# Kernel tuning notes

Measured on AMD Instinct MI355X. Metric: run time of the kernel, lower is better.

## Reference

```python
import jax, jax.numpy as jnp
import numpy as np
import math

BS, N, D_MODEL, H = 8, 1024, 512, 8
D_K = D_MODEL // H


def setup_inputs() -> dict:
    key = jax.random.key(0)
    ks = jax.random.split(key, 12)
    s = 1.0 / math.sqrt(D_MODEL)
    inp = {
        "query": jax.random.normal(ks[0], (BS, N, D_MODEL), jnp.float32),
        "key": jax.random.normal(ks[1], (BS, N, D_MODEL), jnp.float32),
        "value": jax.random.normal(ks[2], (BS, N, D_MODEL), jnp.float32),
        "wc_matrix": jax.random.normal(ks[3], (BS, N, N), jnp.float32),
        "Wq": jax.random.normal(ks[4], (D_MODEL, D_MODEL), jnp.float32) * s,
        "bq": jnp.zeros((D_MODEL,), jnp.float32),
        "Wk": jax.random.normal(ks[5], (D_MODEL, D_MODEL), jnp.float32) * s,
        "bk": jnp.zeros((D_MODEL,), jnp.float32),
        "Wv": jax.random.normal(ks[6], (D_MODEL, D_MODEL), jnp.float32) * s,
        "bv": jnp.zeros((D_MODEL,), jnp.float32),
        "Wo": jax.random.normal(ks[7], (D_MODEL, D_MODEL), jnp.float32) * s,
        "bo": jnp.zeros((D_MODEL,), jnp.float32),
    }
    return inp


def _split_heads(x):
    # (bs, N, d_model) -> (bs, h, N, d_k)
    b, n, _ = x.shape
    return x.reshape(b, n, H, D_K).transpose(0, 2, 1, 3)


def reference(query, key, value, wc_matrix, Wq, bq, Wk, bk, Wv, bv, Wo, bo):
    # Linear projections (torch Linear: x @ W.T + b), split into heads
    q = _split_heads(query @ Wq.T + bq)
    k = _split_heads(key @ Wk.T + bk)
    v = _split_heads(value @ Wv.T + bv)

    # scores: (bs, h, N, N)
    scores = jnp.einsum("bhnd,bhmd->bhnm", q, k) / jnp.sqrt(jnp.float32(D_K))
    # WC modulation: scores * softmax(wc)[:, None] + scores  (softmax_wc=True, residual=True)
    wc_sm = jax.nn.softmax(wc_matrix, axis=-1)[:, None]  # (bs, 1, N, N)
    scores = scores * wc_sm + scores
    p_attn = jax.nn.softmax(scores, axis=-1)  # dropout is identity in eval

    a = jnp.einsum("bhnm,bhmd->bhnd", p_attn, v)
    a = a.transpose(0, 2, 1, 3).reshape(query.shape[0], -1, D_MODEL)
    return a @ Wo.T + bo
```

## Files before the change

### kernel.cpp

```cpp
#include <hip/hip_runtime.h>
#include <math.h>


#define BS 8
#define SEQ 1024
#define DM 512
#define NH 8
#define DK 64
#define ROWS (BS * SEQ)

typedef __bf16 bf16_t;
typedef bf16_t bf16x8 __attribute__((ext_vector_type(8)));
typedef bf16_t bf16x4 __attribute__((ext_vector_type(4)));
typedef float f32x4 __attribute__((ext_vector_type(4)));

__device__ inline f32x4 mfma32(bf16x8 a, bf16x8 b, f32x4 c) {
  return __builtin_amdgcn_mfma_f32_16x16x32_bf16(a, b, c, 0, 0, 0);
}

__device__ inline bf16x8 cvt8(float4 a, float4 b) {
  bf16x8 r;
  r[0] = (bf16_t)a.x; r[1] = (bf16_t)a.y; r[2] = (bf16_t)a.z; r[3] = (bf16_t)a.w;
  r[4] = (bf16_t)b.x; r[5] = (bf16_t)b.y; r[6] = (bf16_t)b.z; r[7] = (bf16_t)b.w;
  return r;
}

__global__ __launch_bounds__(256) void wc_softmax_kernel(const float* __restrict__ wc,
                                                         bf16_t* __restrict__ G) {
  int row = blockIdx.x;
  const float* x = wc + (size_t)row * SEQ;
  bf16_t* y = G + (size_t)row * SEQ;
  int t = threadIdx.x;
  float4 v = *(const float4*)(x + t * 4);
  float m = fmaxf(fmaxf(v.x, v.y), fmaxf(v.z, v.w));
#pragma unroll
  for (int off = 32; off > 0; off >>= 1) m = fmaxf(m, __shfl_xor(m, off, 64));
  __shared__ float sm[4], ss[4];
  int w = t >> 6;
  if ((t & 63) == 0) sm[w] = m;
  __syncthreads();
  m = fmaxf(fmaxf(sm[0], sm[1]), fmaxf(sm[2], sm[3]));
  float4 e;
  e.x = __expf(v.x - m); e.y = __expf(v.y - m);
  e.z = __expf(v.z - m); e.w = __expf(v.w - m);
  float s = e.x + e.y + e.z + e.w;
#pragma unroll
  for (int off = 32; off > 0; off >>= 1) s += __shfl_xor(s, off, 64);
  if ((t & 63) == 0) ss[w] = s;
  __syncthreads();
  s = ss[0] + ss[1] + ss[2] + ss[3];
  float inv = 1.0f / s;
  bf16x4 g;
  g[0] = (bf16_t)(1.0f + e.x * inv);
  g[1] = (bf16_t)(1.0f + e.y * inv);
  g[2] = (bf16_t)(1.0f + e.z * inv);
  g[3] = (bf16_t)(1.0f + e.w * inv);
  *(bf16x4*)(y + t * 4) = g;
}

__global__ __launch_bounds__(256) void gemm_qkv_kernel(
    const float* xq, const float* xk, const float* xv,
    const float* Wq, const float* Wk, const float* Wv,
    const float* bq, const float* bk, const float* bv,
    bf16_t* Cq, bf16_t* Ck, bf16_t* Cv) {
  const float* Xarr[3] = {xq, xk, xv};
  const float* Warr[3] = {Wq, Wk, Wv};
  const float* barr[3] = {bq, bk, bv};
  bf16_t* Carr[3] = {Cq, Ck, Cv};
  int z = blockIdx.z;
  const float* X = Xarr[z];
  const float* W = Warr[z];
  const float* bias = barr[z];
  bf16_t* C = Carr[z];

  __shared__ bf16_t As[128][32];
  __shared__ bf16_t Bs[128][32];
  int t = threadIdx.x;
  int lane = t & 63, w = t >> 6;
  int quad = lane >> 4, l15 = lane & 15;
  int m0w = (w & 1) * 64, n0w = (w >> 1) * 64;
  int mbase = blockIdx.x * 128, nbase = blockIdx.y * 128;
  f32x4 acc[4][4] = {};
  int srow = t >> 1, skoff = (t & 1) * 16;

  for (int kb = 0; kb < DM; kb += 32) {
    const float* p = X + (size_t)(mbase + srow) * DM + kb + skoff;
    float4 x0 = *(const float4*)(p + 0);
    float4 x1 = *(const float4*)(p + 4);
    float4 x2 = *(const float4*)(p + 8);
    float4 x3 = *(const float4*)(p + 12);
    const float* pw = W + (size_t)(nbase + srow) * DM + kb + skoff;
    float4 w0 = *(const float4*)(pw + 0);
    float4 w1 = *(const float4*)(pw + 4);
    float4 w2 = *(const float4*)(pw + 8);
    float4 w3 = *(const float4*)(pw + 12);
    __syncthreads();
    *(bf16x8*)&As[srow][skoff] = cvt8(x0, x1);
    *(bf16x8*)&As[srow][skoff + 8] = cvt8(x2, x3);
    *(bf16x8*)&Bs[srow][skoff] = cvt8(w0, w1);
    *(bf16x8*)&Bs[srow][skoff + 8] = cvt8(w2, w3);
    __syncthreads();
    bf16x8 af[4], bf[4];
#pragma unroll
    for (int mt = 0; mt < 4; ++mt)
      af[mt] = *(const bf16x8*)&As[m0w + mt * 16 + l15][quad * 8];
#pragma unroll
    for (int nt = 0; nt < 4; ++nt)
      bf[nt] = *(const bf16x8*)&Bs[n0w + nt * 16 + l15][quad * 8];
#pragma unroll
    for (int mt = 0; mt < 4; ++mt)
#pragma unroll
      for (int nt = 0; nt < 4; ++nt)
        acc[mt][nt] = mfma32(af[mt], bf[nt], acc[mt][nt]);
  }

#pragma unroll
  for (int nt = 0; nt < 4; ++nt) {
    int col = nbase + n0w + nt * 16 + l15;
    float bc = bias[col];
#pragma unroll
    for (int mt = 0; mt < 4; ++mt)
#pragma unroll
      for (int r = 0; r < 4; ++r) {
        int row = mbase + m0w + mt * 16 + quad * 4 + r;
        C[(size_t)row * DM + col] = (bf16_t)(acc[mt][nt][r] + bc);
      }
  }
}

__global__ __launch_bounds__(256) void gemm_wo_kernel(const bf16_t* __restrict__ X,
                                                      const float* __restrict__ W,
                                                      const float* __restrict__ bias,
                                                      float* __restrict__ C) {
  __shared__ bf16_t As[64][32];
  __shared__ bf16_t Bs[128][32];
  int t = threadIdx.x;
  int lane = t & 63, w = t >> 6;
  int quad = lane >> 4, l15 = lane & 15;
  int m0w = (w & 1) * 32, n0w = (w >> 1) * 64;
  int mbase = blockIdx.x * 64, nbase = blockIdx.y * 128;
  f32x4 acc[2][4] = {};
  int arow = t >> 2, ak8 = (t & 3) * 8;
  int brow = t >> 1, bkoff = (t & 1) * 16;

  for (int kb = 0; kb < DM; kb += 32) {
    bf16x8 xa = *(const bf16x8*)&X[(size_t)(mbase + arow) * DM + kb + ak8];
    const float* pw = W + (size_t)(nbase + brow) * DM + kb + bkoff;
    float4 w0 = *(const float4*)(pw + 0);
    float4 w1 = *(const float4*)(pw + 4);
    float4 w2 = *(const float4*)(pw + 8);
    float4 w3 = *(const float4*)(pw + 12);
    __syncthreads();
    *(bf16x8*)&As[arow][ak8] = xa;
    *(bf16x8*)&Bs[brow][bkoff] = cvt8(w0, w1);
    *(bf16x8*)&Bs[brow][bkoff + 8] = cvt8(w2, w3);
    __syncthreads();
    bf16x8 af[2], bf[4];
#pragma unroll
    for (int mt = 0; mt < 2; ++mt)
      af[mt] = *(const bf16x8*)&As[m0w + mt * 16 + l15][quad * 8];
#pragma unroll
    for (int nt = 0; nt < 4; ++nt)
      bf[nt] = *(const bf16x8*)&Bs[n0w + nt * 16 + l15][quad * 8];
#pragma unroll
    for (int mt = 0; mt < 2; ++mt)
#pragma unroll
      for (int nt = 0; nt < 4; ++nt)
        acc[mt][nt] = mfma32(af[mt], bf[nt], acc[mt][nt]);
  }

#pragma unroll
  for (int nt = 0; nt < 4; ++nt) {
    int col = nbase + n0w + nt * 16 + l15;
    float bc = bias[col];
#pragma unroll
    for (int mt = 0; mt < 2; ++mt)
#pragma unroll
      for (int r = 0; r < 4; ++r) {
        int row = mbase + m0w + mt * 16 + quad * 4 + r;
        C[(size_t)row * DM + col] = acc[mt][nt][r] + bc;
      }
  }
}

__global__ __launch_bounds__(256) void vtrans_kernel(const bf16_t* __restrict__ Vb,
                                                     bf16_t* __restrict__ Vt) {
  int mt = blockIdx.x;
  int bh = blockIdx.y;
  int b = bh >> 3, h = bh & 7;
  __shared__ bf16_t Ts[64][66];
  int t = threadIdx.x;
#pragma unroll
  for (int f = 0; f < 2; ++f) {
    int chunk = t + f * 256;
    int row = chunk >> 3;
    int c8 = (chunk & 7) * 8;
    bf16x8 v = *(const bf16x8*)&Vb[(size_t)(b * SEQ + mt * 64 + row) * DM + h * DK + c8];
#pragma unroll
    for (int j = 0; j < 8; ++j) Ts[c8 + j][row] = v[j];
  }
  __syncthreads();
#pragma unroll
  for (int f = 0; f < 2; ++f) {
    int chunk = t + f * 256;
    int d = chunk >> 3;
    int m8 = (chunk & 7) * 8;
    bf16x8 o;
#pragma unroll
    for (int j = 0; j < 8; ++j) o[j] = Ts[d][m8 + j];
    *(bf16x8*)&Vt[((size_t)(bh * DK + d)) * SEQ + mt * 64 + m8] = o;
  }
}

__global__ __launch_bounds__(256) void flash_mfma_kernel(const bf16_t* __restrict__ Qb,
                                                         const bf16_t* __restrict__ Kb,
                                                         const bf16_t* __restrict__ Vt,
                                                         const bf16_t* __restrict__ G,
                                                         bf16_t* __restrict__ Ab) {
  int qt = blockIdx.x, h = blockIdx.y, b = blockIdx.z;
  __shared__ bf16_t Qs[64][72];
  __shared__ bf16_t Ks[64][72];
  __shared__ bf16_t Vs[64][72];
  __shared__ bf16_t Ps[64][72];
  int t = threadIdx.x, lane = t & 63, w = t >> 6;
  int quad = lane >> 4, l15 = lane & 15;

#pragma unroll
  for (int f = 0; f < 2; ++f) {
    int chunk = t + f * 256;
    int row = chunk >> 3, k8 = (chunk & 7) * 8;
    *(bf16x8*)&Qs[row][k8] =
        *(const bf16x8*)&Qb[(size_t)(b * SEQ + qt * 64 + row) * DM + h * DK + k8];
  }
  __syncthreads();
  bf16x8 aq0 = *(const bf16x8*)&Qs[w * 16 + l15][quad * 8];
  bf16x8 aq1 = *(const bf16x8*)&Qs[w * 16 + l15][32 + quad * 8];

  float m_st = -INFINITY, l_st = 0.f;
  f32x4 o[4] = {};
  const size_t grow = (size_t)(b * SEQ + qt * 64 + w * 16 + l15) * SEQ;

  for (int mt = 0; mt < 16; ++mt) {
    __syncthreads();
#pragma unroll
    for (int f = 0; f < 2; ++f) {
      int chunk = t + f * 256;
      int row = chunk >> 3, k8 = (chunk & 7) * 8;
      *(bf16x8*)&Ks[row][k8] =
          *(const bf16x8*)&Kb[(size_t)(b * SEQ + mt * 64 + row) * DM + h * DK + k8];
      *(bf16x8*)&Vs[row][k8] =
          *(const bf16x8*)&Vt[((size_t)((b * NH + h) * DK + row)) * SEQ + mt * 64 + k8];
    }
    __syncthreads();

    f32x4 s[4];
#pragma unroll
    for (int ct = 0; ct < 4; ++ct) {
      bf16x8 ak0 = *(const bf16x8*)&Ks[ct * 16 + l15][quad * 8];
      bf16x8 ak1 = *(const bf16x8*)&Ks[ct * 16 + l15][32 + quad * 8];
      f32x4 z = {};
      s[ct] = mfma32(ak1, aq1, mfma32(ak0, aq0, z));
    }

    float sv[4][4];
    float rm = -INFINITY;
#pragma unroll
    for (int ct = 0; ct < 4; ++ct) {
      bf16x4 g4 = *(const bf16x4*)&G[grow + mt * 64 + ct * 16 + quad * 4];
#pragma unroll
      for (int r = 0; r < 4; ++r) {
        float x = s[ct][r] * 0.125f * (float)g4[r];
        sv[ct][r] = x;
        rm = fmaxf(rm, x);
      }
    }
    rm = fmaxf(rm, __shfl_xor(rm, 16, 64));
    rm = fmaxf(rm, __shfl_xor(rm, 32, 64));
    float mnew = fmaxf(m_st, rm);
    float alpha = __expf(m_st - mnew);
    m_st = mnew;

    float rs = 0.f;
#pragma unroll
    for (int ct = 0; ct < 4; ++ct) {
      bf16x4 pb;
#pragma unroll
      for (int r = 0; r < 4; ++r) {
        float p = __expf(sv[ct][r] - mnew);
        pb[r] = (bf16_t)p;
        rs += p;
      }
      *(bf16x4*)&Ps[w * 16 + l15][ct * 16 + quad * 4] = pb;
    }
    rs += __shfl_xor(rs, 16, 64);
    rs += __shfl_xor(rs, 32, 64);
    l_st = l_st * alpha + rs;

#pragma unroll
    for (int dt = 0; dt < 4; ++dt) {
      o[dt][0] *= alpha; o[dt][1] *= alpha; o[dt][2] *= alpha; o[dt][3] *= alpha;
    }
#pragma unroll
    for (int c = 0; c < 2; ++c) {
      bf16x8 bp = *(const bf16x8*)&Ps[w * 16 + l15][c * 32 + quad * 8];
#pragma unroll
      for (int dt = 0; dt < 4; ++dt) {
        bf16x8 av = *(const bf16x8*)&Vs[dt * 16 + l15][c * 32 + quad * 8];
        o[dt] = mfma32(av, bp, o[dt]);
      }
    }
  }

  float linv = 1.0f / l_st;
  size_t qrow = (size_t)(b * SEQ + qt * 64 + w * 16 + l15);
#pragma unroll
  for (int dt = 0; dt < 4; ++dt)
#pragma unroll
    for (int r = 0; r < 4; ++r)
      Ab[qrow * DM + h * DK + dt * 16 + quad * 4 + r] = (bf16_t)(o[dt][r] * linv);
}

extern "C" void kernel_launch(void* const* d_in, const int* in_sizes, int n_in,
                              void* d_out, int out_size, void* d_ws, size_t ws_size,
                              hipStream_t stream) {
  const float* query = (const float*)d_in[0];
  const float* key = (const float*)d_in[1];
  const float* value = (const float*)d_in[2];
  const float* wc = (const float*)d_in[3];
  const float* Wq = (const float*)d_in[4];
  const float* bq = (const float*)d_in[5];
  const float* Wk = (const float*)d_in[6];
  const float* bk = (const float*)d_in[7];
  const float* Wv = (const float*)d_in[8];
  const float* bv = (const float*)d_in[9];
  const float* Wo = (const float*)d_in[10];
  const float* bo = (const float*)d_in[11];
  float* out = (float*)d_out;

  bf16_t* Qb = (bf16_t*)d_ws;
  bf16_t* Kb = Qb + (size_t)ROWS * DM;
  bf16_t* Vb = Kb + (size_t)ROWS * DM;
  bf16_t* Vt = Vb + (size_t)ROWS * DM;
  bf16_t* Ab = Vt + (size_t)ROWS * DM;
  bf16_t* G = Ab + (size_t)ROWS * DM;

  wc_softmax_kernel<<<BS * SEQ, 256, 0, stream>>>(wc, G);

  gemm_qkv_kernel<<<dim3(ROWS / 128, DM / 128, 3), 256, 0, stream>>>(
      query, key, value, Wq, Wk, Wv, bq, bk, bv, Qb, Kb, Vb);

  vtrans_kernel<<<dim3(16, 64), 256, 0, stream>>>(Vb, Vt);

  flash_mfma_kernel<<<dim3(SEQ / 64, NH, BS), 256, 0, stream>>>(Qb, Kb, Vt, G, Ab);

  gemm_wo_kernel<<<dim3(ROWS / 64, DM / 128), 256, 0, stream>>>(Ab, Wo, bo, out);
}
```

Measured before the change: 257.4 us.

## Pre-convert inputs and weights to bf16 and stage GEMM tiles via direct global-to-LDS loads

A new conversion kernel turns query/key/value and all four weight matrices to bf16 in workspace. The QKV and output GEMMs then share a templated core that loads bf16 tiles straight into LDS with global_load_lds instead of loading fp32 into registers, converting, and storing. This removes per-tile conversion work and register staging, and the fp32 weights are no longer re-read and re-converted by every block. The cost is an extra pass that reads fp32 activations and writes bf16 copies, which adds memory traffic and a launch.

```diff
diff --git a/kernel.cpp b/kernel.cpp
--- a/kernel.cpp
+++ b/kernel.cpp
@@ -18,11 +18,34 @@
   return __builtin_amdgcn_mfma_f32_16x16x32_bf16(a, b, c, 0, 0, 0);
 }
 
-__device__ inline bf16x8 cvt8(float4 a, float4 b) {
-  bf16x8 r;
-  r[0] = (bf16_t)a.x; r[1] = (bf16_t)a.y; r[2] = (bf16_t)a.z; r[3] = (bf16_t)a.w;
-  r[4] = (bf16_t)b.x; r[5] = (bf16_t)b.y; r[6] = (bf16_t)b.z; r[7] = (bf16_t)b.w;
-  return r;
+__device__ inline void gload_lds16(const bf16_t* g, bf16_t* l) {
+  __builtin_amdgcn_global_load_lds(
+      (const __attribute__((address_space(1))) void*)g,
+      (__attribute__((address_space(3))) void*)l, 16, 0, 0);
+}
+
+__global__ __launch_bounds__(256) void cvt_kernel(
+    const float* q, const float* k, const float* v,
+    const float* wq, const float* wk, const float* wv, const float* wo,
+    bf16_t* xq, bf16_t* xk, bf16_t* xv,
+    bf16_t* wqb, bf16_t* wkb, bf16_t* wvb, bf16_t* wob) {
+  const float* srcs[7] = {q, k, v, wq, wk, wv, wo};
+  bf16_t* dsts[7] = {xq, xk, xv, wqb, wkb, wvb, wob};
+  int b = blockIdx.x;
+  int seg, boff;
+  if (b < 1536) { seg = b >> 9; boff = b & 511; }
+  else { seg = 3 + ((b - 1536) >> 5); boff = (b - 1536) & 31; }
+  const float* src = srcs[seg] + (size_t)boff * 8192;
+  bf16_t* dst = dsts[seg] + (size_t)boff * 8192;
+  int t = threadIdx.x;
+#pragma unroll
+  for (int f = 0; f < 8; ++f) {
+    int idx = (f * 256 + t) * 4;
+    float4 x = *(const float4*)(src + idx);
+    bf16x4 o;
+    o[0] = (bf16_t)x.x; o[1] = (bf16_t)x.y; o[2] = (bf16_t)x.z; o[3] = (bf16_t)x.w;
+    *(bf16x4*)(dst + idx) = o;
+  }
 }
 
 __global__ __launch_bounds__(256) void wc_softmax_kernel(const float* __restrict__ wc,
@@ -58,57 +81,42 @@
   *(bf16x4*)(y + t * 4) = g;
 }
 
-__global__ __launch_bounds__(256) void gemm_qkv_kernel(
-    const float* xq, const float* xk, const float* xv,
-    const float* Wq, const float* Wk, const float* Wv,
-    const float* bq, const float* bk, const float* bv,
-    bf16_t* Cq, bf16_t* Ck, bf16_t* Cv) {
-  const float* Xarr[3] = {xq, xk, xv};
-  const float* Warr[3] = {Wq, Wk, Wv};
-  const float* barr[3] = {bq, bk, bv};
-  bf16_t* Carr[3] = {Cq, Ck, Cv};
-  int z = blockIdx.z;
-  const float* X = Xarr[z];
-  const float* W = Warr[z];
-  const float* bias = barr[z];
-  bf16_t* C = Carr[z];
-
-  __shared__ bf16_t As[128][32];
-  __shared__ bf16_t Bs[128][32];
-  int t = threadIdx.x;
-  int lane = t & 63, w = t >> 6;
+template <int BM, bool OUTF32>
+__device__ inline void gemm_core(const bf16_t* X, const bf16_t* W,
+                                 const float* bias, void* Cv,
+                                 int mblk, int nblk) {
+  __shared__ bf16_t As[BM * 32];
+  __shared__ bf16_t Bs[128 * 32];
+  int t = threadIdx.x, lane = t & 63, w = t >> 6;
   int quad = lane >> 4, l15 = lane & 15;
-  int m0w = (w & 1) * 64, n0w = (w >> 1) * 64;
-  int mbase = blockIdx.x * 128, nbase = blockIdx.y * 128;
-  f32x4 acc[4][4] = {};
-  int srow = t >> 1, skoff = (t & 1) * 16;
+  constexpr int MT = BM / 32;
+  int m0w = (w & 1) * (BM / 2), n0w = (w >> 1) * 64;
+  int mbase = mblk * BM, nbase = nblk * 128;
+  int lr = lane >> 2, l4 = lane & 3;
+  f32x4 acc[MT][4] = {};
 
   for (int kb = 0; kb < DM; kb += 32) {
-    const float* p = X + (size_t)(mbase + srow) * DM + kb + skoff;
-    float4 x0 = *(const float4*)(p + 0);
-    float4 x1 = *(const float4*)(p + 4);
-    float4 x2 = *(const float4*)(p + 8);
-    float4 x3 = *(const float4*)(p + 12);
-    const float* pw = W + (size_t)(nbase + srow) * DM + kb + skoff;
-    float4 w0 = *(const float4*)(pw + 0);
-    float4 w1 = *(const float4*)(pw + 4);
-    float4 w2 = *(const float4*)(pw + 8);
-    float4 w3 = *(const float4*)(pw + 12);
     __syncthreads();
-    *(bf16x8*)&As[srow][skoff] = cvt8(x0, x1);
-    *(bf16x8*)&As[srow][skoff + 8] = cvt8(x2, x3);
-    *(bf16x8*)&Bs[srow][skoff] = cvt8(w0, w1);
-    *(bf16x8*)&Bs[srow][skoff + 8] = cvt8(w2, w3);
+#pragma unroll
+    for (int f = 0; f < BM / 64; ++f) {
+      int i = f * 4 + w;
+      gload_lds16(X + (size_t)(mbase + i * 16 + lr) * DM + kb + l4 * 8, As + i * 512);
+    }
+#pragma unroll
+    for (int f = 0; f < 2; ++f) {
+      int i = f * 4 + w;
+      gload_lds16(W + (size_t)(nbase + i * 16 + lr) * DM + kb + l4 * 8, Bs + i * 512);
+    }
     __syncthreads();
-    bf16x8 af[4], bf[4];
-#pragma unroll
-    for (int mt = 0; mt < 4; ++mt)
-      af[mt] = *(const bf16x8*)&As[m0w + mt * 16 + l15][quad * 8];
+    bf16x8 af[MT], bf[4];
+#pragma unroll
+    for (int mt = 0; mt < MT; ++mt)
+      af[mt] = *(const bf16x8*)&As[(m0w + mt * 16 + l15) * 32 + quad * 8];
 #pragma unroll
     for (int nt = 0; nt < 4; ++nt)
-      bf[nt] = *(const bf16x8*)&Bs[n0w + nt * 16 + l15][quad * 8];
-#pragma unroll
-    for (int mt = 0; mt < 4; ++mt)
+      bf[nt] = *(const bf16x8*)&Bs[(n0w + nt * 16 + l15) * 32 + quad * 8];
+#pragma unroll
+    for (int mt = 0; mt < MT; ++mt)
 #pragma unroll
       for (int nt = 0; nt < 4; ++nt)
         acc[mt][nt] = mfma32(af[mt], bf[nt], acc[mt][nt]);
@@ -119,68 +127,35 @@
     int col = nbase + n0w + nt * 16 + l15;
     float bc = bias[col];
 #pragma unroll
-    for (int mt = 0; mt < 4; ++mt)
+    for (int mt = 0; mt < MT; ++mt)
 #pragma unroll
       for (int r = 0; r < 4; ++r) {
         int row = mbase + m0w + mt * 16 + quad * 4 + r;
-        C[(size_t)row * DM + col] = (bf16_t)(acc[mt][nt][r] + bc);
+        float vv = acc[mt][nt][r] + bc;
+        if (OUTF32)
+          ((float*)Cv)[(size_t)row * DM + col] = vv;
+        else
+          ((bf16_t*)Cv)[(size_t)row * DM + col] = (bf16_t)vv;
       }
   }
 }
 
-__global__ __launch_bounds__(256) void gemm_wo_kernel(const bf16_t* __restrict__ X,
-                                                      const float* __restrict__ W,
-                                                      const float* __restrict__ bias,
-                                                      float* __restrict__ C) {
-  __shared__ bf16_t As[64][32];
-  __shared__ bf16_t Bs[128][32];
-  int t = threadIdx.x;
-  int lane = t & 63, w = t >> 6;
-  int quad = lane >> 4, l15 = lane & 15;
-  int m0w = (w & 1) * 32, n0w = (w >> 1) * 64;
-  int mbase = blockIdx.x * 64, nbase = blockIdx.y * 128;
-  f32x4 acc[2][4] = {};
-  int arow = t >> 2, ak8 = (t & 3) * 8;
-  int brow = t >> 1, bkoff = (t & 1) * 16;
-
-  for (int kb = 0; kb < DM; kb += 32) {
-    bf16x8 xa = *(const bf16x8*)&X[(size_t)(mbase + arow) * DM + kb + ak8];
-    const float* pw = W + (size_t)(nbase + brow) * DM + kb + bkoff;
-    float4 w0 = *(const float4*)(pw + 0);
-    float4 w1 = *(const float4*)(pw + 4);
-    float4 w2 = *(const float4*)(pw + 8);
-    float4 w3 = *(const float4*)(pw + 12);
-    __syncthreads();
-    *(bf16x8*)&As[arow][ak8] = xa;
-    *(bf16x8*)&Bs[brow][bkoff] = cvt8(w0, w1);
-    *(bf16x8*)&Bs[brow][bkoff + 8] = cvt8(w2, w3);
-    __syncthreads();
-    bf16x8 af[2], bf[4];
-#pragma unroll
-    for (int mt = 0; mt < 2; ++mt)
-      af[mt] = *(const bf16x8*)&As[m0w + mt * 16 + l15][quad * 8];
-#pragma unroll
-    for (int nt = 0; nt < 4; ++nt)
-      bf[nt] = *(const bf16x8*)&Bs[n0w + nt * 16 + l15][quad * 8];
-#pragma unroll
-    for (int mt = 0; mt < 2; ++mt)
-#pragma unroll
-      for (int nt = 0; nt < 4; ++nt)
-        acc[mt][nt] = mfma32(af[mt], bf[nt], acc[mt][nt]);
-  }
-
-#pragma unroll
-  for (int nt = 0; nt < 4; ++nt) {
-    int col = nbase + n0w + nt * 16 + l15;
-    float bc = bias[col];
-#pragma unroll
-    for (int mt = 0; mt < 2; ++mt)
-#pragma unroll
-      for (int r = 0; r < 4; ++r) {
-        int row = mbase + m0w + mt * 16 + quad * 4 + r;
-        C[(size_t)row * DM + col] = acc[mt][nt][r] + bc;
-      }
-  }
+__global__ __launch_bounds__(256) void gemm_qkv_kernel(
+    const bf16_t* xq, const bf16_t* xk, const bf16_t* xv,
+    const bf16_t* wq, const bf16_t* wk, const bf16_t* wv,
+    const float* bq, const float* bk, const float* bv,
+    bf16_t* cq, bf16_t* ck, bf16_t* cv) {
+  const bf16_t* Xarr[3] = {xq, xk, xv};
+  const bf16_t* Warr[3] = {wq, wk, wv};
+  const float* barr[3] = {bq, bk, bv};
+  bf16_t* Carr[3] = {cq, ck, cv};
+  int z = blockIdx.z;
+  gemm_core<128, false>(Xarr[z], Warr[z], barr[z], Carr[z], blockIdx.x, blockIdx.y);
+}
+
+__global__ __launch_bounds__(256) void gemm_wo_kernel(const bf16_t* X, const bf16_t* W,
+                                                      const float* bias, float* C) {
+  gemm_core<64, true>(X, W, bias, C, blockIdx.x, blockIdx.y);
 }
 
 __global__ __launch_bounds__(256) void vtrans_kernel(const bf16_t* __restrict__ Vb,
@@ -337,21 +312,33 @@
   const float* bo = (const float*)d_in[11];
   float* out = (float*)d_out;
 
+  const size_t ACT = (size_t)ROWS * DM;
+  const size_t WSZ = (size_t)DM * DM;
   bf16_t* Qb = (bf16_t*)d_ws;
-  bf16_t* Kb = Qb + (size_t)ROWS * DM;
-  bf16_t* Vb = Kb + (size_t)ROWS * DM;
-  bf16_t* Vt = Vb + (size_t)ROWS * DM;
-  bf16_t* Ab = Vt + (size_t)ROWS * DM;
-  bf16_t* G = Ab + (size_t)ROWS * DM;
+  bf16_t* Kb = Qb + ACT;
+  bf16_t* Vb = Kb + ACT;
+  bf16_t* Vt = Vb + ACT;
+  bf16_t* Ab = Vt + ACT;
+  bf16_t* G = Ab + ACT;
+  bf16_t* Xq = G + (size_t)BS * SEQ * SEQ;
+  bf16_t* Xk = Xq + ACT;
+  bf16_t* Xv = Xk + ACT;
+  bf16_t* Wqb = Xv + ACT;
+  bf16_t* Wkb = Wqb + WSZ;
+  bf16_t* Wvb = Wkb + WSZ;
+  bf16_t* Wob = Wvb + WSZ;
+
+  cvt_kernel<<<1664, 256, 0, stream>>>(query, key, value, Wq, Wk, Wv, Wo,
+                                       Xq, Xk, Xv, Wqb, Wkb, Wvb, Wob);
 
   wc_softmax_kernel<<<BS * SEQ, 256, 0, stream>>>(wc, G);
 
   gemm_qkv_kernel<<<dim3(ROWS / 128, DM / 128, 3), 256, 0, stream>>>(
-      query, key, value, Wq, Wk, Wv, bq, bk, bv, Qb, Kb, Vb);
+      Xq, Xk, Xv, Wqb, Wkb, Wvb, bq, bk, bv, Qb, Kb, Vb);
 
   vtrans_kernel<<<dim3(16, 64), 256, 0, stream>>>(Vb, Vt);
 
   flash_mfma_kernel<<<dim3(SEQ / 64, NH, BS), 256, 0, stream>>>(Qb, Kb, Vt, G, Ab);
 
-  gemm_wo_kernel<<<dim3(ROWS / 64, DM / 128), 256, 0, stream>>>(Ab, Wo, bo, out);
-}
+  gemm_wo_kernel<<<dim3(ROWS / 64, DM / 128), 256, 0, stream>>>(Ab, Wob, bo, out);
+}
```

New measurement: 241.3 us. 6.2% less time.
